# Kernel optimization log

Measured on AMD Instinct MI355X. Metric: run time of the kernel, lower is better.

The kernel has to match this reference:

```python
import jax, jax.numpy as jnp
import numpy as np

BETA = 0.25

def setup_inputs() -> dict:
    key = jax.random.key(0)
    k1, k2 = jax.random.split(key)
    z = jax.random.normal(k1, (4096, 64, 64), dtype=jnp.float32)
    codebooks = jax.random.normal(k2, (64, 256, 64), dtype=jnp.float32)
    return {"z": z, "codebooks": codebooks}

def reference(z, codebooks):
    # z: (B, M, d); codebooks: (M, K, d)
    B, M, d = z.shape
    # squared distances (B, M, K) via ||z||^2 - 2 z.c + ||c||^2 (avoids (B,M,K,d) blowup)
    z2 = jnp.sum(z * z, axis=-1)                      # (B, M)
    c2 = jnp.sum(codebooks * codebooks, axis=-1)      # (M, K)
    zc = jnp.einsum('bmd,mkd->bmk', z, codebooks)     # (B, M, K)
    distances = z2[:, :, None] - 2.0 * zc + c2[None]  # (B, M, K)
    encoding_indices = jnp.argmin(distances, axis=-1) # (B, M) int
    # per-subspace codebook gather: codebooks[m, idx[b, m], :]
    quantized_raw = codebooks[jnp.arange(M)[None, :], encoding_indices]  # (B, M, d)
    # straight-through estimator
    quantized = z + jax.lax.stop_gradient(quantized_raw - z)
    q_loss = (BETA * jnp.mean((jax.lax.stop_gradient(quantized) - z) ** 2)
              + jnp.mean((quantized - jax.lax.stop_gradient(z)) ** 2))
    return quantized, encoding_indices, q_loss
```

## Files before the change

### kernel.cpp

```cpp
#include <hip/hip_runtime.h>

#define IDX_BASE 16777216UL
#define LOSS_IDX 17039360UL
#define EPS2 0.02f

typedef float4 f4;
typedef _Float16 half8 __attribute__((ext_vector_type(8)));
typedef float f32x4 __attribute__((ext_vector_type(4)));

__device__ __forceinline__ void gload_lds16(const float* g, float* s) {
    __builtin_amdgcn_global_load_lds(
        (const __attribute__((address_space(1))) unsigned int*)g,
        (__attribute__((address_space(3))) unsigned int*)s, 16, 0, 0);
}

__global__ __launch_bounds__(256) void pq_c2(const float* __restrict__ cb,
                                             float* __restrict__ c2) {
    int m = blockIdx.x, k = threadIdx.x;
    const f4* row = reinterpret_cast<const f4*>(cb + ((size_t)m * 256 + k) * 64);
    float s0 = 0.f, s1 = 0.f;
    #pragma unroll
    for (int i = 0; i < 16; i += 2) {
        f4 a = row[i], b = row[i + 1];
        s0 = fmaf(a.x,a.x,s0); s0 = fmaf(a.y,a.y,s0); s0 = fmaf(a.z,a.z,s0); s0 = fmaf(a.w,a.w,s0);
        s1 = fmaf(b.x,b.x,s1); s1 = fmaf(b.y,b.y,s1); s1 = fmaf(b.z,b.z,s1); s1 = fmaf(b.w,b.w,s1);
    }
    c2[m * 256 + k] = s0 + s1;
}

__global__ __launch_bounds__(256) void pq_frag(const float* __restrict__ cb,
                                               half8* __restrict__ fragbuf) {
    int m = blockIdx.x, tid = threadIdx.x;
    int w = tid >> 6, lane = tid & 63, lh = lane >> 4, l15 = lane & 15;
    const float* cbm = cb + (size_t)m * (256 * 64);
    half8* fbm = fragbuf + (size_t)m * (16 * 4 * 64);
    #pragma unroll
    for (int ti = 0; ti < 4; ++ti) {
        int tile = w * 4 + ti;
        int code = tile * 16 + l15;
        const float* crow = cbm + code * 64 + lh * 8;
        #pragma unroll
        for (int s = 0; s < 2; ++s) {
            f4 a = *reinterpret_cast<const f4*>(crow + s * 32);
            f4 b = *reinterpret_cast<const f4*>(crow + s * 32 + 4);
            float v[8] = {a.x, a.y, a.z, a.w, b.x, b.y, b.z, b.w};
            half8 hi, lo;
            #pragma unroll
            for (int e = 0; e < 8; ++e) {
                _Float16 h = (_Float16)v[e];
                hi[e] = h; lo[e] = (_Float16)(v[e] - (float)h);
            }
            fbm[(tile * 4 + s * 2 + 0) * 64 + lane] = hi;
            fbm[(tile * 4 + s * 2 + 1) * 64 + lane] = lo;
        }
    }
}

__global__ __launch_bounds__(256, 3) void pq_main(
    const float* __restrict__ z, const float* __restrict__ cb,
    const float* __restrict__ c2ws, const half8* __restrict__ fragbuf,
    float* __restrict__ out, float* __restrict__ partial)
{
    __shared__ f4    sZ4[128 * 16];
    __shared__ float sM1[4 * 128];
    __shared__ float sM2[4 * 128];
    __shared__ int   sK [4 * 128];
    __shared__ int   sBest[128];
    __shared__ float sW[4];

    const int tid = threadIdx.x, bx = blockIdx.x;
    const int m = ((bx & 7) << 3) | ((bx >> 3) & 7);
    const int chunk = bx >> 6;
    const int w = tid >> 6, lane = tid & 63;
    const int lh = lane >> 4, l15 = lane & 15;

    const float* __restrict__ cbm = cb + (size_t)m * (256 * 64);
    const f4* cb4m = reinterpret_cast<const f4*>(cbm);

    #pragma unroll
    for (int i = 0; i < 8; ++i) {
        int unit = i * 256 + w * 64 + lane;
        int row = unit >> 4, c4 = unit & 15;
        int c4p = c4 ^ (row & 7);
        const float* src = z + ((size_t)(chunk * 128 + row) * 64 + m) * 64 + c4p * 4;
        gload_lds16(src, (float*)&sZ4[i * 256 + w * 64]);
    }

    const half8* __restrict__ fb = fragbuf + (size_t)m * (16 * 4 * 64);
    half8 ah[4][2], al[4][2];
    #pragma unroll
    for (int t = 0; t < 4; ++t) {
        #pragma unroll
        for (int s = 0; s < 2; ++s) {
            ah[t][s] = fb[((w * 4 + t) * 4 + s * 2 + 0) * 64 + lane];
            al[t][s] = fb[((w * 4 + t) * 4 + s * 2 + 1) * 64 + lane];
        }
    }
    const f4* __restrict__ c2t = reinterpret_cast<const f4*>(c2ws + m * 256);
    f32x4 c2i[4];
    #pragma unroll
    for (int t = 0; t < 4; ++t) {
        f4 cv = c2t[(w * 4 + t) * 4 + lh];
        c2i[t][0] = -0.5f*cv.x; c2i[t][1] = -0.5f*cv.y;
        c2i[t][2] = -0.5f*cv.z; c2i[t][3] = -0.5f*cv.w;
    }

    __syncthreads();

    #pragma unroll 1
    for (int rtp = 0; rtp < 4; ++rtp) {
        half8 bh0[2], bl0[2], bh1[2], bl1[2];
        #pragma unroll
        for (int h = 0; h < 2; ++h) {
            const int row = (rtp * 2 + h) * 16 + l15;
            const int swz = row & 7;
            const f4* zr = &sZ4[row * 16];
            const int c0 = lh << 1;
            f4 a0 = zr[(c0)     ^ swz];
            f4 a1 = zr[(c0 + 1) ^ swz];
            f4 a2 = zr[(c0 + 8) ^ swz];
            f4 a3 = zr[(c0 + 9) ^ swz];
            float v0[8] = {a0.x,a0.y,a0.z,a0.w,a1.x,a1.y,a1.z,a1.w};
            float v1[8] = {a2.x,a2.y,a2.z,a2.w,a3.x,a3.y,a3.z,a3.w};
            #pragma unroll
            for (int e = 0; e < 8; ++e) {
                _Float16 h0 = (_Float16)v0[e];
                bh0[h][e] = h0; bl0[h][e] = (_Float16)(v0[e] - (float)h0);
                _Float16 h1 = (_Float16)v1[e];
                bh1[h][e] = h1; bl1[h][e] = (_Float16)(v1[e] - (float)h1);
            }
        }
        float m1[2] = {-1e30f, -1e30f}, m2[2] = {-1e30f, -1e30f};
        int k16[2] = {0, 0};
        #pragma unroll
        for (int t = 0; t < 4; ++t) {
            #pragma unroll
            for (int h = 0; h < 2; ++h) {
                f32x4 acc = c2i[t];
                acc = __builtin_amdgcn_mfma_f32_16x16x32_f16(ah[t][0], bh0[h], acc, 0, 0, 0);
                acc = __builtin_amdgcn_mfma_f32_16x16x32_f16(ah[t][1], bh1[h], acc, 0, 0, 0);
                acc = __builtin_amdgcn_mfma_f32_16x16x32_f16(ah[t][0], bl0[h], acc, 0, 0, 0);
                acc = __builtin_amdgcn_mfma_f32_16x16x32_f16(ah[t][1], bl1[h], acc, 0, 0, 0);
                acc = __builtin_amdgcn_mfma_f32_16x16x32_f16(al[t][0], bh0[h], acc, 0, 0, 0);
                acc = __builtin_amdgcn_mfma_f32_16x16x32_f16(al[t][1], bh1[h], acc, 0, 0, 0);
                #pragma unroll
                for (int r = 0; r < 4; ++r) {
                    float v = acc[r];
                    m2[h] = __builtin_amdgcn_fmed3f(v, m1[h], m2[h]);
                    bool gt = v > m1[h];
                    m1[h]  = gt ? v : m1[h];
                    k16[h] = gt ? (t * 16 + r) : k16[h];
                }
            }
        }
        #pragma unroll
        for (int h = 0; h < 2; ++h) {
            int kw = k16[h] + lh * 4;
            float a1v = m1[h], a2v = m2[h];
            #pragma unroll
            for (int off = 16; off <= 32; off <<= 1) {
                float om1 = __shfl_xor(a1v, off, 64);
                float om2 = __shfl_xor(a2v, off, 64);
                int   okw = __shfl_xor(kw, off, 64);
                a2v = fmaxf(fmaxf(a2v, om2), fminf(a1v, om1));
                bool better = (om1 > a1v) || (om1 == a1v && okw < kw);
                a1v = better ? om1 : a1v;
                kw  = better ? okw : kw;
            }
            if (lane < 16) {
                int r2 = (rtp * 2 + h) * 16 + lane;
                sM1[w * 128 + r2] = a1v;
                sM2[w * 128 + r2] = a2v;
                sK [w * 128 + r2] = kw;
            }
        }
    }
    __syncthreads();

    if (tid < 128) {
        float M1 = -1e30f, M2 = -1e30f; int K1 = 0;
        #pragma unroll
        for (int w2 = 0; w2 < 4; ++w2) {
            float v1 = sM1[w2 * 128 + tid];
            float v2 = sM2[w2 * 128 + tid];
            int   kk = w2 * 64 + sK[w2 * 128 + tid];
            M2 = fmaxf(fmaxf(M2, v2), fminf(M1, v1));
            bool better = v1 > M1;
            M1 = better ? v1 : M1;
            K1 = better ? kk : K1;
        }
        sBest[tid] = (M1 - M2 < EPS2) ? -1 : K1;
    }
    __syncthreads();

    for (int row = w; row < 128; row += 4) {
        if (sBest[row] >= 0) continue;
        int swz = row & 7;
        float bs = -1e30f; int bk = 0;
        #pragma unroll 1
        for (int j = 0; j < 4; ++j) {
            int k = j * 64 + lane;
            float s = -0.5f * c2ws[m * 256 + k];
            #pragma unroll
            for (int d4 = 0; d4 < 16; ++d4) {
                f4 cvv = cb4m[k * 16 + d4];
                f4 zz  = sZ4[row * 16 + (d4 ^ swz)];
                s = fmaf(zz.x, cvv.x, s); s = fmaf(zz.y, cvv.y, s);
                s = fmaf(zz.z, cvv.z, s); s = fmaf(zz.w, cvv.w, s);
            }
            if (s > bs) { bs = s; bk = k; }
        }
        #pragma unroll
        for (int off = 1; off < 64; off <<= 1) {
            float ov = __shfl_xor(bs, off, 64);
            int   ok = __shfl_xor(bk, off, 64);
            if (ov > bs || (ov == bs && ok < bk)) { bs = ov; bk = ok; }
        }
        if (lane == 0) sBest[row] = bk;
    }
    __syncthreads();

    float lsum = 0.f;
    {
        int row = tid >> 1, h = tid & 1;
        int k = sBest[row];
        int b = chunk * 128 + row;
        int swz = row & 7;
        const f4* q4 = cb4m + (size_t)k * 16 + h * 8;
        f4*       o4 = reinterpret_cast<f4*>(out + ((size_t)b * 64 + m) * 64) + h * 8;
        float l0 = 0.f, l1 = 0.f;
        #pragma unroll
        for (int c = 0; c < 8; ++c) {
            f4 qv = q4[c];
            f4 zv = sZ4[row * 16 + (((h << 3) + c) ^ swz)];
            o4[c] = qv;
            float d0 = qv.x - zv.x, d1 = qv.y - zv.y, d2 = qv.z - zv.z, d3 = qv.w - zv.w;
            l0 = fmaf(d0, d0, l0); l1 = fmaf(d1, d1, l1);
            l0 = fmaf(d2, d2, l0); l1 = fmaf(d3, d3, l1);
        }
        lsum = l0 + l1;
    }
    if (tid < 128)
        out[IDX_BASE + (size_t)(chunk * 128 + tid) * 64 + m] = (float)sBest[tid];
    #pragma unroll
    for (int off = 1; off < 64; off <<= 1) lsum += __shfl_xor(lsum, off, 64);
    if (lane == 0) sW[w] = lsum;
    __syncthreads();
    if (tid == 0) partial[bx] = (sW[0] + sW[1]) + (sW[2] + sW[3]);
}

__global__ __launch_bounds__(256) void pq_loss(const float* __restrict__ partial,
                                               float* __restrict__ out)
{
    __shared__ float sW[4];
    float s = 0.f;
    #pragma unroll
    for (int i = 0; i < 8; ++i) s += partial[threadIdx.x + i * 256];
    #pragma unroll
    for (int off = 1; off < 64; off <<= 1) s += __shfl_xor(s, off, 64);
    if ((threadIdx.x & 63) == 0) sW[threadIdx.x >> 6] = s;
    __syncthreads();
    if (threadIdx.x == 0)
        out[LOSS_IDX] = ((sW[0] + sW[1]) + (sW[2] + sW[3])) * (1.25f / 16777216.0f);
}

extern "C" void kernel_launch(void* const* d_in, const int* in_sizes, int n_in,
                              void* d_out, int out_size, void* d_ws, size_t ws_size,
                              hipStream_t stream) {
    const float* zp  = (const float*)d_in[0];
    const float* cbp = (const float*)d_in[1];
    float* outp = (float*)d_out;
    float* c2ws = (float*)d_ws;
    half8* frag = (half8*)((float*)d_ws + 16384);
    float* part = (float*)d_ws + 16384 + 1048576;

    pq_c2  <<<dim3(64),   dim3(256), 0, stream>>>(cbp, c2ws);
    pq_frag<<<dim3(64),   dim3(256), 0, stream>>>(cbp, frag);
    pq_main<<<dim3(2048), dim3(256), 0, stream>>>(zp, cbp, c2ws, frag, outp, part);
    pq_loss<<<dim3(1),    dim3(256), 0, stream>>>(part, outp);
}
```

Before: 89.40 us.

## Pack score and index into sortable uint keys; fuse codebook norms into frag kernel

Replaces the float max/second-max plus index tracking in the MFMA epilogue with monotone-uint keys that carry the code index in their low 8 bits. This lets top-2 selection use plain umax/umin networks and halves the shuffle and LDS traffic in the reductions. It also folds the codebook squared-norm computation into the fragment-building kernel, which now runs on 256 blocks, removing one launch. Dropping the low 8 mantissa bits slightly coarsens the scores used for the margin test, and the fallback exact path covers ambiguous rows.

```diff
diff --git a/kernel.cpp b/kernel.cpp
--- a/kernel.cpp
+++ b/kernel.cpp
@@ -7,6 +7,16 @@
 typedef float4 f4;
 typedef _Float16 half8 __attribute__((ext_vector_type(8)));
 typedef float f32x4 __attribute__((ext_vector_type(4)));
+
+static __device__ __forceinline__ unsigned umax(unsigned a, unsigned b) { return a > b ? a : b; }
+static __device__ __forceinline__ unsigned umin(unsigned a, unsigned b) { return a < b ? a : b; }
+static __device__ __forceinline__ unsigned f2mono(float s) {
+    unsigned u = __float_as_uint(s);
+    return u ^ (unsigned)(((int)u >> 31) | 0x80000000);
+}
+static __device__ __forceinline__ float mono2f(unsigned v) {
+    return __uint_as_float(v ^ (((unsigned)((int)(~v) >> 31)) | 0x80000000u));
+}
 
 __device__ __forceinline__ void gload_lds16(const float* g, float* s) {
     __builtin_amdgcn_global_load_lds(
@@ -14,46 +24,36 @@
         (__attribute__((address_space(3))) unsigned int*)s, 16, 0, 0);
 }
 
-__global__ __launch_bounds__(256) void pq_c2(const float* __restrict__ cb,
-                                             float* __restrict__ c2) {
-    int m = blockIdx.x, k = threadIdx.x;
-    const f4* row = reinterpret_cast<const f4*>(cb + ((size_t)m * 256 + k) * 64);
-    float s0 = 0.f, s1 = 0.f;
-    #pragma unroll
-    for (int i = 0; i < 16; i += 2) {
-        f4 a = row[i], b = row[i + 1];
-        s0 = fmaf(a.x,a.x,s0); s0 = fmaf(a.y,a.y,s0); s0 = fmaf(a.z,a.z,s0); s0 = fmaf(a.w,a.w,s0);
-        s1 = fmaf(b.x,b.x,s1); s1 = fmaf(b.y,b.y,s1); s1 = fmaf(b.z,b.z,s1); s1 = fmaf(b.w,b.w,s1);
-    }
-    c2[m * 256 + k] = s0 + s1;
-}
-
 __global__ __launch_bounds__(256) void pq_frag(const float* __restrict__ cb,
-                                               half8* __restrict__ fragbuf) {
-    int m = blockIdx.x, tid = threadIdx.x;
+                                               half8* __restrict__ fragbuf,
+                                               float* __restrict__ c2) {
+    int bx = blockIdx.x, tid = threadIdx.x;
+    int m = bx >> 2, sub = bx & 3;
     int w = tid >> 6, lane = tid & 63, lh = lane >> 4, l15 = lane & 15;
     const float* cbm = cb + (size_t)m * (256 * 64);
     half8* fbm = fragbuf + (size_t)m * (16 * 4 * 64);
-    #pragma unroll
-    for (int ti = 0; ti < 4; ++ti) {
-        int tile = w * 4 + ti;
-        int code = tile * 16 + l15;
-        const float* crow = cbm + code * 64 + lh * 8;
-        #pragma unroll
-        for (int s = 0; s < 2; ++s) {
-            f4 a = *reinterpret_cast<const f4*>(crow + s * 32);
-            f4 b = *reinterpret_cast<const f4*>(crow + s * 32 + 4);
-            float v[8] = {a.x, a.y, a.z, a.w, b.x, b.y, b.z, b.w};
-            half8 hi, lo;
-            #pragma unroll
-            for (int e = 0; e < 8; ++e) {
-                _Float16 h = (_Float16)v[e];
-                hi[e] = h; lo[e] = (_Float16)(v[e] - (float)h);
-            }
-            fbm[(tile * 4 + s * 2 + 0) * 64 + lane] = hi;
-            fbm[(tile * 4 + s * 2 + 1) * 64 + lane] = lo;
-        }
-    }
+    int tile = w * 4 + sub;
+    int code = tile * 16 + l15;
+    const float* crow = cbm + code * 64 + lh * 8;
+    float ss = 0.f;
+    #pragma unroll
+    for (int s = 0; s < 2; ++s) {
+        f4 a = *reinterpret_cast<const f4*>(crow + s * 32);
+        f4 b = *reinterpret_cast<const f4*>(crow + s * 32 + 4);
+        float v[8] = {a.x, a.y, a.z, a.w, b.x, b.y, b.z, b.w};
+        half8 hi, lo;
+        #pragma unroll
+        for (int e = 0; e < 8; ++e) {
+            _Float16 h = (_Float16)v[e];
+            hi[e] = h; lo[e] = (_Float16)(v[e] - (float)h);
+            ss = fmaf(v[e], v[e], ss);
+        }
+        fbm[(tile * 4 + s * 2 + 0) * 64 + lane] = hi;
+        fbm[(tile * 4 + s * 2 + 1) * 64 + lane] = lo;
+    }
+    ss += __shfl_xor(ss, 16, 64);
+    ss += __shfl_xor(ss, 32, 64);
+    if (lh == 0) c2[m * 256 + code] = ss;
 }
 
 __global__ __launch_bounds__(256, 3) void pq_main(
@@ -61,18 +61,18 @@
     const float* __restrict__ c2ws, const half8* __restrict__ fragbuf,
     float* __restrict__ out, float* __restrict__ partial)
 {
-    __shared__ f4    sZ4[128 * 16];
-    __shared__ float sM1[4 * 128];
-    __shared__ float sM2[4 * 128];
-    __shared__ int   sK [4 * 128];
-    __shared__ int   sBest[128];
-    __shared__ float sW[4];
+    __shared__ f4       sZ4[128 * 16];
+    __shared__ unsigned sK1[4 * 128];
+    __shared__ unsigned sK2[4 * 128];
+    __shared__ int      sBest[128];
+    __shared__ float    sW[4];
 
     const int tid = threadIdx.x, bx = blockIdx.x;
     const int m = ((bx & 7) << 3) | ((bx >> 3) & 7);
     const int chunk = bx >> 6;
     const int w = tid >> 6, lane = tid & 63;
     const int lh = lane >> 4, l15 = lane & 15;
+    const unsigned payBase = 255u - (unsigned)(w * 64 + lh * 4);
 
     const float* __restrict__ cbm = cb + (size_t)m * (256 * 64);
     const f4* cb4m = reinterpret_cast<const f4*>(cbm);
@@ -130,10 +130,10 @@
                 bh1[h][e] = h1; bl1[h][e] = (_Float16)(v1[e] - (float)h1);
             }
         }
-        float m1[2] = {-1e30f, -1e30f}, m2[2] = {-1e30f, -1e30f};
-        int k16[2] = {0, 0};
+        unsigned K1[2] = {0u, 0u}, K2[2] = {0u, 0u};
         #pragma unroll
         for (int t = 0; t < 4; ++t) {
+            const unsigned pb = payBase - (unsigned)(t * 16);
             #pragma unroll
             for (int h = 0; h < 2; ++h) {
                 f32x4 acc = c2i[t];
@@ -143,53 +143,48 @@
                 acc = __builtin_amdgcn_mfma_f32_16x16x32_f16(ah[t][1], bl1[h], acc, 0, 0, 0);
                 acc = __builtin_amdgcn_mfma_f32_16x16x32_f16(al[t][0], bh0[h], acc, 0, 0, 0);
                 acc = __builtin_amdgcn_mfma_f32_16x16x32_f16(al[t][1], bh1[h], acc, 0, 0, 0);
-                #pragma unroll
-                for (int r = 0; r < 4; ++r) {
-                    float v = acc[r];
-                    m2[h] = __builtin_amdgcn_fmed3f(v, m1[h], m2[h]);
-                    bool gt = v > m1[h];
-                    m1[h]  = gt ? v : m1[h];
-                    k16[h] = gt ? (t * 16 + r) : k16[h];
-                }
+                unsigned kk0 = (f2mono(acc[0]) & 0xFFFFFF00u) | (pb - 0u);
+                unsigned kk1 = (f2mono(acc[1]) & 0xFFFFFF00u) | (pb - 1u);
+                unsigned kk2 = (f2mono(acc[2]) & 0xFFFFFF00u) | (pb - 2u);
+                unsigned kk3 = (f2mono(acc[3]) & 0xFFFFFF00u) | (pb - 3u);
+                unsigned a  = umax(kk0, kk1), b2 = umin(kk0, kk1);
+                unsigned c  = umax(kk2, kk3), d  = umin(kk2, kk3);
+                unsigned t1 = umax(a, c);
+                unsigned t2 = umax(umin(a, c), umax(b2, d));
+                K2[h] = umax(umax(K2[h], t2), umin(K1[h], t1));
+                K1[h] = umax(K1[h], t1);
             }
         }
         #pragma unroll
         for (int h = 0; h < 2; ++h) {
-            int kw = k16[h] + lh * 4;
-            float a1v = m1[h], a2v = m2[h];
             #pragma unroll
             for (int off = 16; off <= 32; off <<= 1) {
-                float om1 = __shfl_xor(a1v, off, 64);
-                float om2 = __shfl_xor(a2v, off, 64);
-                int   okw = __shfl_xor(kw, off, 64);
-                a2v = fmaxf(fmaxf(a2v, om2), fminf(a1v, om1));
-                bool better = (om1 > a1v) || (om1 == a1v && okw < kw);
-                a1v = better ? om1 : a1v;
-                kw  = better ? okw : kw;
+                unsigned o1 = (unsigned)__shfl_xor((int)K1[h], off, 64);
+                unsigned o2 = (unsigned)__shfl_xor((int)K2[h], off, 64);
+                K2[h] = umax(umax(K2[h], o2), umin(K1[h], o1));
+                K1[h] = umax(K1[h], o1);
             }
             if (lane < 16) {
                 int r2 = (rtp * 2 + h) * 16 + lane;
-                sM1[w * 128 + r2] = a1v;
-                sM2[w * 128 + r2] = a2v;
-                sK [w * 128 + r2] = kw;
+                sK1[w * 128 + r2] = K1[h];
+                sK2[w * 128 + r2] = K2[h];
             }
         }
     }
     __syncthreads();
 
     if (tid < 128) {
-        float M1 = -1e30f, M2 = -1e30f; int K1 = 0;
+        unsigned G1 = 0u, G2 = 0u;
         #pragma unroll
         for (int w2 = 0; w2 < 4; ++w2) {
-            float v1 = sM1[w2 * 128 + tid];
-            float v2 = sM2[w2 * 128 + tid];
-            int   kk = w2 * 64 + sK[w2 * 128 + tid];
-            M2 = fmaxf(fmaxf(M2, v2), fminf(M1, v1));
-            bool better = v1 > M1;
-            M1 = better ? v1 : M1;
-            K1 = better ? kk : K1;
-        }
-        sBest[tid] = (M1 - M2 < EPS2) ? -1 : K1;
+            unsigned k1w = sK1[w2 * 128 + tid];
+            unsigned k2w = sK2[w2 * 128 + tid];
+            G2 = umax(umax(G2, k2w), umin(G1, k1w));
+            G1 = umax(G1, k1w);
+        }
+        float s1 = mono2f(G1 & 0xFFFFFF00u);
+        float s2 = mono2f(G2 & 0xFFFFFF00u);
+        sBest[tid] = (s1 - s2 < EPS2) ? -1 : (int)(255u - (G1 & 0xFFu));
     }
     __syncthreads();
 
@@ -274,8 +269,7 @@
     half8* frag = (half8*)((float*)d_ws + 16384);
     float* part = (float*)d_ws + 16384 + 1048576;
 
-    pq_c2  <<<dim3(64),   dim3(256), 0, stream>>>(cbp, c2ws);
-    pq_frag<<<dim3(64),   dim3(256), 0, stream>>>(cbp, frag);
+    pq_frag<<<dim3(256),  dim3(256), 0, stream>>>(cbp, frag, c2ws);
     pq_main<<<dim3(2048), dim3(256), 0, stream>>>(zp, cbp, c2ws, frag, outp, part);
     pq_loss<<<dim3(1),    dim3(256), 0, stream>>>(part, outp);
 }
```

Measured after the change: 84.58 us. 5.4% less time.
